# Kernel optimization log

Hardware: AMD Instinct MI355X
Metric: run time of the kernel (lower is better)

The kernel has to match this reference:

```python
import jax, jax.numpy as jnp
import numpy as np

NUM_GROUPS = 8
EPS = 1e-5


def group_norm(x, gamma, beta):
    # x: [B, C, H, W]
    B, C, H, W = x.shape
    xg = x.reshape(B, NUM_GROUPS, C // NUM_GROUPS, H, W)
    mean = xg.mean(axis=(2, 3, 4), keepdims=True)
    var = xg.var(axis=(2, 3, 4), keepdims=True)
    xn = ((xg - mean) * jax.lax.rsqrt(var + EPS)).reshape(B, C, H, W)
    return xn * gamma[None, :, None, None] + beta[None, :, None, None]


def conv1x1(x, w, b):
    # x: [B, C, H, W], w: [Cout, Cin], b: [Cout]
    return jnp.einsum('bchw,oc->bohw', x, w) + b[None, :, None, None]


def setup_inputs() -> dict:
    key = jax.random.key(0)
    ks = jax.random.split(key, 7)
    C = 128
    x = jax.random.normal(ks[0], (4, C, 64, 64), dtype=jnp.float32)
    norm_w = jnp.ones((C,), dtype=jnp.float32)
    norm_b = jnp.zeros((C,), dtype=jnp.float32)
    s = 1.0 / np.sqrt(C)
    qkv_w = jax.random.normal(ks[1], (3 * C, C), dtype=jnp.float32) * s
    qkv_b = jax.random.normal(ks[2], (3 * C,), dtype=jnp.float32) * 0.01
    proj_w = jax.random.normal(ks[3], (C, C), dtype=jnp.float32) * s
    proj_b = jax.random.normal(ks[4], (C,), dtype=jnp.float32) * 0.01
    return {"x": x, "norm_w": norm_w, "norm_b": norm_b,
            "qkv_w": qkv_w, "qkv_b": qkv_b,
            "proj_w": proj_w, "proj_b": proj_b}


def reference(x, norm_w, norm_b, qkv_w, qkv_b, proj_w, proj_b):
    B, C, H, W = x.shape
    qkv = conv1x1(group_norm(x, norm_w, norm_b), qkv_w, qkv_b)
    q, k, v = jnp.split(qkv, 3, axis=1)           # each [B, C, H, W]
    q = q.reshape(B, C, H * W).transpose(0, 2, 1)  # [B, HW, C]
    k = k.reshape(B, C, H * W)                     # [B, C, HW]
    v = v.reshape(B, C, H * W).transpose(0, 2, 1)  # [B, HW, C]
    scale = 1.0 / np.sqrt(C).astype(np.float32)
    attn = jax.nn.softmax(jnp.einsum('bnc,bcm->bnm', q, k) * scale, axis=-1)
    out = jnp.einsum('bnm,bmc->bnc', attn, v)      # [B, HW, C]
    out = out.transpose(0, 2, 1).reshape(B, C, H, W)
    return x + conv1x1(out, proj_w, proj_b)
```

## Files before the change

kernel.cpp:

```cpp
#include <hip/hip_runtime.h>

typedef unsigned short u16;
typedef unsigned int   u32;

#define HW 4096
#define NC 128

typedef __bf16 bf16x8 __attribute__((ext_vector_type(8)));
typedef float  f32x16 __attribute__((ext_vector_type(16)));

__device__ __forceinline__ bf16x8 as_bf8(uint4 u){
    union { uint4 u; bf16x8 b; } c; c.u = u; return c.b;
}
__device__ __forceinline__ u16 f2bf(float f){
    u32 u = __float_as_uint(f);
    return (u16)((u + 0x7fffu + ((u >> 16) & 1u)) >> 16);
}
__device__ __forceinline__ u32 pack2(float a, float b){
    return ((__float_as_uint(a) + 0x8000u) >> 16) | ((__float_as_uint(b) + 0x8000u) & 0xffff0000u);
}
__device__ __forceinline__ float bf_lo(u32 u){ return __uint_as_float(u << 16); }
__device__ __forceinline__ float bf_hi(u32 u){ return __uint_as_float(u & 0xffff0000u); }
__device__ __forceinline__ void unpack8(uint4 u, float* v){
    v[0]=bf_lo(u.x); v[1]=bf_hi(u.x); v[2]=bf_lo(u.y); v[3]=bf_hi(u.y);
    v[4]=bf_lo(u.z); v[5]=bf_hi(u.z); v[6]=bf_lo(u.w); v[7]=bf_hi(u.w);
}

#define GLOAD_LDS16(g, l) \
    __builtin_amdgcn_global_load_lds((const __attribute__((address_space(1))) u32*)(const void*)(g), \
                                     (__attribute__((address_space(3))) u32*)(void*)(l), 16, 0, 0)

__global__ __launch_bounds__(256) void gnw_kernel(const float* __restrict__ x,
                                                  float* __restrict__ stats,
                                                  const float* __restrict__ qkv_w,
                                                  const float* __restrict__ proj_w,
                                                  uint4* __restrict__ Wf,
                                                  uint4* __restrict__ Pf){
    if (blockIdx.x < 256){
        int bg = blockIdx.x >> 3, part = blockIdx.x & 7;
        const float4* p = (const float4*)(x + (size_t)bg * 65536 + part * 8192);
        float s = 0.f, ss = 0.f;
        #pragma unroll
        for (int i = 0; i < 8; i++){
            float4 u = p[threadIdx.x + i*256];
            s  += u.x + u.y + u.z + u.w;
            ss += u.x*u.x + u.y*u.y + u.z*u.z + u.w*u.w;
        }
        #pragma unroll
        for (int off = 32; off > 0; off >>= 1){
            s  += __shfl_xor(s,  off);
            ss += __shfl_xor(ss, off);
        }
        __shared__ float rs[4], rss[4];
        int wid = threadIdx.x >> 6;
        if ((threadIdx.x & 63) == 0){ rs[wid] = s; rss[wid] = ss; }
        __syncthreads();
        if (threadIdx.x == 0){
            stats[bg*16 + part*2]     = rs[0]+rs[1]+rs[2]+rs[3];
            stats[bg*16 + part*2 + 1] = rss[0]+rss[1]+rss[2]+rss[3];
        }
    } else {
        int id = (blockIdx.x - 256)*256 + threadIdx.x;
        const float* src; uint4* dst; int fi;
        if (id < 6144){ src = qkv_w; dst = Wf; fi = id; }
        else          { src = proj_w; dst = Pf; fi = id - 6144; }
        int l = fi & 63, ks = (fi >> 6) & 7, ob = fi >> 9;
        int o = ob*32 + (l & 31);
        int c = ks*16 + ((l >> 5) << 3);
        const float* s = src + o*128 + c;
        dst[fi] = make_uint4(pack2(s[0],s[1]), pack2(s[2],s[3]), pack2(s[4],s[5]), pack2(s[6],s[7]));
    }
}

__global__ __launch_bounds__(256) void qkv_kernel(const float* __restrict__ x,
                                                  const float* __restrict__ stats,
                                                  const float* __restrict__ gamma,
                                                  const float* __restrict__ beta,
                                                  const uint4* __restrict__ Wf,
                                                  const float* __restrict__ bias,
                                                  uint4* __restrict__ Qf,
                                                  uint4* __restrict__ Kf,
                                                  uint4* __restrict__ Vf){
    __shared__ float gaL[128], beL[128], biasL[384];
    int b = blockIdx.x >> 7, tokblk = blockIdx.x & 127;
    int t = threadIdx.x, lane = t & 63, wv = t >> 6;
    if (t < 128){
        int g = t >> 4;
        float S = 0.f, SS = 0.f;
        #pragma unroll
        for (int p = 0; p < 8; p++){
            S  += stats[(b*8 + g)*16 + p*2];
            SS += stats[(b*8 + g)*16 + p*2 + 1];
        }
        float mean = S * (1.f/65536.f);
        float rstd = rsqrtf(SS * (1.f/65536.f) - mean*mean + 1e-5f);
        float ga = gamma[t] * rstd;
        gaL[t] = ga; beL[t] = beta[t] - mean*ga;
    }
    if (t < 192){ biasL[t] = bias[t]; biasL[t+192] = bias[t+192]; }
    __syncthreads();

    int h = lane >> 5, tl = lane & 31;
    uint4 xf[8];
    const float* xb = x + (size_t)b*128*HW + tokblk*32 + tl;
    #pragma unroll
    for (int ks = 0; ks < 8; ks++){
        int c0 = ks*16 + h*8;
        float4 g0 = *(float4*)&gaL[c0], g1 = *(float4*)&gaL[c0+4];
        float4 e0 = *(float4*)&beL[c0], e1 = *(float4*)&beL[c0+4];
        float v[8];
        #pragma unroll
        for (int j = 0; j < 8; j++) v[j] = xb[(size_t)(c0+j)*HW];
        v[0] = fmaf(v[0], g0.x, e0.x); v[1] = fmaf(v[1], g0.y, e0.y);
        v[2] = fmaf(v[2], g0.z, e0.z); v[3] = fmaf(v[3], g0.w, e0.w);
        v[4] = fmaf(v[4], g1.x, e1.x); v[5] = fmaf(v[5], g1.y, e1.y);
        v[6] = fmaf(v[6], g1.z, e1.z); v[7] = fmaf(v[7], g1.w, e1.w);
        xf[ks] = make_uint4(pack2(v[0],v[1]), pack2(v[2],v[3]), pack2(v[4],v[5]), pack2(v[6],v[7]));
    }

    bool up = (lane >= 32);
    #pragma unroll
    for (int i = 0; i < 3; i++){
        int ob = wv*3 + i;
        uint4 wf[8];
        #pragma unroll
        for (int ks = 0; ks < 8; ks++) wf[ks] = Wf[(ob*8 + ks)*64 + lane];
        f32x16 D;
        #pragma unroll
        for (int r = 0; r < 16; r++) D[r] = 0.f;
        if (ob < 8){
            #pragma unroll
            for (int ks = 0; ks < 8; ks++)
                D = __builtin_amdgcn_mfma_f32_32x32x16_bf16(as_bf8(wf[ks]), as_bf8(xf[ks]), D, 0,0,0);
            #pragma unroll
            for (int r = 0; r < 16; r++)
                D[r] += biasL[ob*32 + (r&3) + 8*(r>>2) + 4*h];
            u32 pk[8], xch[8];
            #pragma unroll
            for (int j = 0; j < 8; j++) pk[j] = pack2(D[2*j], D[2*j+1]);
            #pragma unroll
            for (int j = 0; j < 8; j++) xch[j] = __shfl_xor(pk[j], 32);
            uint4 F0 = up ? make_uint4(xch[2],xch[3],pk[2],pk[3]) : make_uint4(pk[0],pk[1],xch[0],xch[1]);
            uint4 F1 = up ? make_uint4(xch[6],xch[7],pk[6],pk[7]) : make_uint4(pk[4],pk[5],xch[4],xch[5]);
            uint4* dst = (ob < 4) ? Qf : Kf;
            int obl = ob & 3;
            size_t base = (((size_t)b*128 + tokblk)*8 + obl*2)*64 + lane;
            dst[base] = F0; dst[base + 64] = F1;
        } else {
            #pragma unroll
            for (int ks = 0; ks < 8; ks++)
                D = __builtin_amdgcn_mfma_f32_32x32x16_bf16(as_bf8(xf[ks]), as_bf8(wf[ks]), D, 0,0,0);
            int nb = ob - 8;
            float vb = biasL[256 + nb*32 + tl];
            #pragma unroll
            for (int r = 0; r < 16; r++) D[r] += vb;
            u32 pk[8], xch[8];
            #pragma unroll
            for (int j = 0; j < 8; j++) pk[j] = pack2(D[2*j], D[2*j+1]);
            #pragma unroll
            for (int j = 0; j < 8; j++) xch[j] = __shfl_xor(pk[j], 32);
            uint4 F0 = up ? make_uint4(xch[2],xch[3],pk[2],pk[3]) : make_uint4(pk[0],pk[1],xch[0],xch[1]);
            uint4 F1 = up ? make_uint4(xch[6],xch[7],pk[6],pk[7]) : make_uint4(pk[4],pk[5],xch[4],xch[5]);
            int it = tokblk >> 1, t2 = tokblk & 1;
            size_t base = ((((size_t)b*64 + it)*4 + nb)*4 + t2*2)*64 + lane;
            Vf[base] = F0; Vf[base + 64] = F1;
        }
    }
}

__global__ __launch_bounds__(256, 2) void attn_kernel(const uint4* __restrict__ Qf,
                                                      const uint4* __restrict__ Kf,
                                                      const uint4* __restrict__ Vf,
                                                      u16* __restrict__ Opart,
                                                      float* __restrict__ lsum){
    __shared__ uint4 smem[2048];
    __shared__ float lred[64];
    int pair = blockIdx.x & 7, qx = blockIdx.x >> 3;
    int b = pair >> 1, ksp = pair & 1;
    int t = threadIdx.x, lane = t & 63, wv = t >> 6;
    int qh = wv >> 1, kh = wv & 1;
    const float SC = 0.08838834764831845f;

    uint4 qf[8];
    const uint4* qptr = Qf + ((size_t)b*128 + qx*2 + qh)*512 + lane;
    #pragma unroll
    for (int ks = 0; ks < 8; ks++) qf[ks] = qptr[ks*64];

    f32x16 O0, O1, O2, O3;
    #pragma unroll
    for (int r = 0; r < 16; r++){ O0[r]=0.f; O1[r]=0.f; O2[r]=0.f; O3[r]=0.f; }
    float l_i = 0.f;

    const uint4* kg = Kf + ((size_t)b*128 + ksp*64)*512;
    const uint4* vg = Vf + ((size_t)b*64  + ksp*32)*1024;

    #pragma unroll
    for (int i = 0; i < 4; i++)
        GLOAD_LDS16(kg + t + i*256, &smem[t + i*256]);
    __syncthreads();

    for (int it = 0; it < 32; it++){
        int cur = it & 1;
        if (it < 31){
            const uint4* kg2 = kg + (it+1)*1024;
            #pragma unroll
            for (int i = 0; i < 4; i++)
                GLOAD_LDS16(kg2 + t + i*256, &smem[(cur^1)*1024 + t + i*256]);
        }
        const uint4* vgi = vg + it*1024 + lane;
        uint4 vf[8];
        #pragma unroll
        for (int nb = 0; nb < 4; nb++){
            vf[nb*2]   = vgi[(nb*4 + kh*2)     << 6];
            vf[nb*2+1] = vgi[(nb*4 + kh*2 + 1) << 6];
        }

        f32x16 S0;
        #pragma unroll
        for (int r = 0; r < 16; r++) S0[r] = 0.f;
        #pragma unroll
        for (int ks = 0; ks < 8; ks++)
            S0 = __builtin_amdgcn_mfma_f32_32x32x16_bf16(
                     as_bf8(smem[cur*1024 + ((kh*8 + ks)<<6) + lane]),
                     as_bf8(qf[ks]), S0, 0,0,0);

        float psum = 0.f;
        u32 pk[8];
        #pragma unroll
        for (int q = 0; q < 4; q++){
            float e0 = __expf(__fmaf_rn(S0[q*4+0], SC, -8.f));
            float e1 = __expf(__fmaf_rn(S0[q*4+1], SC, -8.f));
            float e2 = __expf(__fmaf_rn(S0[q*4+2], SC, -8.f));
            float e3 = __expf(__fmaf_rn(S0[q*4+3], SC, -8.f));
            psum += (e0+e1)+(e2+e3);
            pk[2*q] = pack2(e0,e1); pk[2*q+1] = pack2(e2,e3);
        }
        psum += __shfl_xor(psum, 32);
        l_i += psum;

        u32 xch[8];
        #pragma unroll
        for (int i = 0; i < 8; i++) xch[i] = __shfl_xor(pk[i], 32);
        bool up = (lane >= 32);
        uint4 fr0 = up ? make_uint4(xch[2],xch[3],pk[2],pk[3]) : make_uint4(pk[0],pk[1],xch[0],xch[1]);
        uint4 fr1 = up ? make_uint4(xch[6],xch[7],pk[6],pk[7]) : make_uint4(pk[4],pk[5],xch[4],xch[5]);

        #pragma unroll
        for (int ks = 0; ks < 2; ks++){
            bf16x8 pa = as_bf8(ks ? fr1 : fr0);
            O0 = __builtin_amdgcn_mfma_f32_32x32x16_bf16(pa, as_bf8(vf[0*2+ks]), O0, 0,0,0);
            O1 = __builtin_amdgcn_mfma_f32_32x32x16_bf16(pa, as_bf8(vf[1*2+ks]), O1, 0,0,0);
            O2 = __builtin_amdgcn_mfma_f32_32x32x16_bf16(pa, as_bf8(vf[2*2+ks]), O2, 0,0,0);
            O3 = __builtin_amdgcn_mfma_f32_32x32x16_bf16(pa, as_bf8(vf[3*2+ks]), O3, 0,0,0);
        }
        __syncthreads();
    }

    float* fsm = (float*)smem;
    if (kh == 1){
        #pragma unroll
        for (int r = 0; r < 16; r++){
            fsm[((qh*4+0)*16 + r)*64 + lane] = O0[r];
            fsm[((qh*4+1)*16 + r)*64 + lane] = O1[r];
            fsm[((qh*4+2)*16 + r)*64 + lane] = O2[r];
            fsm[((qh*4+3)*16 + r)*64 + lane] = O3[r];
        }
        if (lane < 32) lred[qh*32 + lane] = l_i;
    }
    __syncthreads();
    if (kh == 0){
        float lt = l_i + lred[qh*32 + (lane & 31)];
        if (lane < 32) lsum[((size_t)(ksp*4 + b))*HW + qx*64 + qh*32 + lane] = lt;
        u16* ob = Opart + (((size_t)(ksp*4 + b))*HW + qx*64 + qh*32)*NC;
        #pragma unroll
        for (int r = 0; r < 16; r++){
            int qr = (r&3) + 8*(r>>2) + 4*(lane>>5);
            int c  = lane & 31;
            ob[qr*NC +      c] = f2bf(O0[r] + fsm[((qh*4+0)*16 + r)*64 + lane]);
            ob[qr*NC + 32 + c] = f2bf(O1[r] + fsm[((qh*4+1)*16 + r)*64 + lane]);
            ob[qr*NC + 64 + c] = f2bf(O2[r] + fsm[((qh*4+2)*16 + r)*64 + lane]);
            ob[qr*NC + 96 + c] = f2bf(O3[r] + fsm[((qh*4+3)*16 + r)*64 + lane]);
        }
    }
}

__global__ __launch_bounds__(256) void proj_kernel(const u16* __restrict__ Op,
                                                   const float* __restrict__ lsum,
                                                   const uint4* __restrict__ Pf,
                                                   const float* __restrict__ bias,
                                                   const float* __restrict__ x,
                                                   float* __restrict__ out){
    __shared__ float biasL[128];
    int t = threadIdx.x, lane = t & 63, wv = t >> 6;
    if (t < 128) biasL[t] = bias[t];
    __syncthreads();
    int b = blockIdx.x >> 6, tk = blockIdx.x & 63;
    int tokb2 = wv & 1, obh = wv >> 1;
    int tokblk = tk*2 + tokb2;
    int h = lane >> 5, tl = lane & 31;

    int rowg = b*HW + tokblk*32 + tl;
    float inv = 1.f / (lsum[rowg] + lsum[16384 + rowg]);
    const u16* p0 = Op + (size_t)rowg*NC + h*8;
    uint4 af[8];
    #pragma unroll
    for (int ks = 0; ks < 8; ks++){
        uint4 u0 = *(const uint4*)(p0 + ks*16);
        uint4 u1 = *(const uint4*)(p0 + 2097152 + ks*16);
        float v0[8], v1[8];
        unpack8(u0, v0); unpack8(u1, v1);
        u32 q[4];
        #pragma unroll
        for (int j = 0; j < 4; j++)
            q[j] = pack2((v0[2*j] + v1[2*j]) * inv, (v0[2*j+1] + v1[2*j+1]) * inv);
        af[ks] = make_uint4(q[0], q[1], q[2], q[3]);
    }

    #pragma unroll
    for (int i = 0; i < 2; i++){
        int ob = obh*2 + i;
        uint4 pf[8];
        #pragma unroll
        for (int ks = 0; ks < 8; ks++) pf[ks] = Pf[(ob*8 + ks)*64 + lane];
        f32x16 D;
        #pragma unroll
        for (int r = 0; r < 16; r++) D[r] = 0.f;
        #pragma unroll
        for (int ks = 0; ks < 8; ks++)
            D = __builtin_amdgcn_mfma_f32_32x32x16_bf16(as_bf8(pf[ks]), as_bf8(af[ks]), D, 0,0,0);
        #pragma unroll
        for (int r = 0; r < 16; r++){
            int o = ob*32 + (r&3) + 8*(r>>2) + 4*h;
            size_t gi = ((size_t)b*128 + o)*HW + tokblk*32 + tl;
            out[gi] = x[gi] + biasL[o] + D[r];
        }
    }
}

extern "C" void kernel_launch(void* const* d_in, const int* in_sizes, int n_in,
                              void* d_out, int out_size, void* d_ws, size_t ws_size,
                              hipStream_t stream){
    const float* x      = (const float*)d_in[0];
    const float* norm_w = (const float*)d_in[1];
    const float* norm_b = (const float*)d_in[2];
    const float* qkv_w  = (const float*)d_in[3];
    const float* qkv_b  = (const float*)d_in[4];
    const float* proj_w = (const float*)d_in[5];
    const float* proj_b = (const float*)d_in[6];
    float* out = (float*)d_out;

    char* w = (char*)d_ws;
    float* stats = (float*)w;
    uint4* Qf = (uint4*)(w + 2048);
    uint4* Kf = (uint4*)(w + 2048 + 4194304);
    uint4* Vf = (uint4*)(w + 2048 + 8388608);
    float* lsum = (float*)(w + 2048 + 12582912);
    uint4* Wf = (uint4*)(w + 2048 + 12582912 + 131072);
    uint4* Pf = (uint4*)(w + 2048 + 12582912 + 131072 + 98304);
    u16* Opart = (u16*)d_out;

    gnw_kernel<<<288, 256, 0, stream>>>(x, stats, qkv_w, proj_w, Wf, Pf);
    qkv_kernel<<<512, 256, 0, stream>>>(x, stats, norm_w, norm_b, Wf, qkv_b, Qf, Kf, Vf);
    attn_kernel<<<512, 256, 0, stream>>>(Qf, Kf, Vf, Opart, lsum);
    proj_kernel<<<256, 256, 0, stream>>>(Opart, lsum, Pf, proj_b, x, out);
}
```

Before: 141.0 us.

## Load K directly to registers, use exp2, and write fragment-layout partial outputs

The attention kernel drops the LDS double buffer for K and its per-iteration barrier. Each wave now loads its own K and V fragments straight into registers and prefetches the next tile after use. The QK accumulation is split into two independent MFMA chains, and the exponential uses the hardware exp2 with folded scale and bias constants. Partial outputs are written as packed MFMA-fragment uint4 tiles rather than scattered 16-bit stores, and the projection kernel reads them with coalesced vector loads. The cost is higher register pressure and exposed global-load latency without LDS staging.

Result: faster. 135.3 us (-4.0%).

```diff
diff --git a/kernel.cpp b/kernel.cpp
--- a/kernel.cpp
+++ b/kernel.cpp
@@ -26,9 +26,7 @@
     v[4]=bf_lo(u.z); v[5]=bf_hi(u.z); v[6]=bf_lo(u.w); v[7]=bf_hi(u.w);
 }
 
-#define GLOAD_LDS16(g, l) \
-    __builtin_amdgcn_global_load_lds((const __attribute__((address_space(1))) u32*)(const void*)(g), \
-                                     (__attribute__((address_space(3))) u32*)(void*)(l), 16, 0, 0)
+__device__ __forceinline__ float exp2_hw(float x){ return __builtin_amdgcn_exp2f(x); }
 
 __global__ __launch_bounds__(256) void gnw_kernel(const float* __restrict__ x,
                                                   float* __restrict__ stats,
@@ -171,67 +169,68 @@
 __global__ __launch_bounds__(256, 2) void attn_kernel(const uint4* __restrict__ Qf,
                                                       const uint4* __restrict__ Kf,
                                                       const uint4* __restrict__ Vf,
-                                                      u16* __restrict__ Opart,
+                                                      uint4* __restrict__ Opart,
                                                       float* __restrict__ lsum){
-    __shared__ uint4 smem[2048];
+    __shared__ float fsm[8192];
     __shared__ float lred[64];
     int pair = blockIdx.x & 7, qx = blockIdx.x >> 3;
     int b = pair >> 1, ksp = pair & 1;
     int t = threadIdx.x, lane = t & 63, wv = t >> 6;
     int qh = wv >> 1, kh = wv & 1;
-    const float SC = 0.08838834764831845f;
+    const float SC2 = 0.12751744361402804f;
+    const float B2  = -11.541560327111707f;
 
     uint4 qf[8];
-    const uint4* qptr = Qf + ((size_t)b*128 + qx*2 + qh)*512 + lane;
+    const uint4* qptr = Qf + (((size_t)b*128 + qx*2 + qh)*8)*64 + lane;
     #pragma unroll
     for (int ks = 0; ks < 8; ks++) qf[ks] = qptr[ks*64];
 
-    f32x16 O0, O1, O2, O3;
-    #pragma unroll
-    for (int r = 0; r < 16; r++){ O0[r]=0.f; O1[r]=0.f; O2[r]=0.f; O3[r]=0.f; }
+    f32x16 O[4];
+    #pragma unroll
+    for (int nb = 0; nb < 4; nb++)
+        #pragma unroll
+        for (int r = 0; r < 16; r++) O[nb][r] = 0.f;
     float l_i = 0.f;
 
-    const uint4* kg = Kf + ((size_t)b*128 + ksp*64)*512;
-    const uint4* vg = Vf + ((size_t)b*64  + ksp*32)*1024;
-
-    #pragma unroll
-    for (int i = 0; i < 4; i++)
-        GLOAD_LDS16(kg + t + i*256, &smem[t + i*256]);
-    __syncthreads();
+    const uint4* kgw = Kf + (((size_t)b*128 + ksp*64)*8)*64 + (kh<<9) + lane;
+    const uint4* vgw = Vf + (((size_t)b*64  + ksp*32)*16)*64 + (kh<<7) + lane;
+
+    uint4 kf[8], vf[8];
+    #pragma unroll
+    for (int ks = 0; ks < 8; ks++) kf[ks] = kgw[ks*64];
+    #pragma unroll
+    for (int nb = 0; nb < 4; nb++){
+        vf[nb*2]   = vgw[nb*256];
+        vf[nb*2+1] = vgw[nb*256 + 64];
+    }
 
     for (int it = 0; it < 32; it++){
-        int cur = it & 1;
+        f32x16 Sa, Sb;
+        #pragma unroll
+        for (int r = 0; r < 16; r++){ Sa[r] = 0.f; Sb[r] = 0.f; }
+        #pragma unroll
+        for (int ks = 0; ks < 4; ks++)
+            Sa = __builtin_amdgcn_mfma_f32_32x32x16_bf16(as_bf8(kf[ks]), as_bf8(qf[ks]), Sa, 0,0,0);
+        #pragma unroll
+        for (int ks = 4; ks < 8; ks++)
+            Sb = __builtin_amdgcn_mfma_f32_32x32x16_bf16(as_bf8(kf[ks]), as_bf8(qf[ks]), Sb, 0,0,0);
+        #pragma unroll
+        for (int r = 0; r < 16; r++) Sa[r] += Sb[r];
+
         if (it < 31){
-            const uint4* kg2 = kg + (it+1)*1024;
-            #pragma unroll
-            for (int i = 0; i < 4; i++)
-                GLOAD_LDS16(kg2 + t + i*256, &smem[(cur^1)*1024 + t + i*256]);
-        }
-        const uint4* vgi = vg + it*1024 + lane;
-        uint4 vf[8];
-        #pragma unroll
-        for (int nb = 0; nb < 4; nb++){
-            vf[nb*2]   = vgi[(nb*4 + kh*2)     << 6];
-            vf[nb*2+1] = vgi[(nb*4 + kh*2 + 1) << 6];
-        }
-
-        f32x16 S0;
-        #pragma unroll
-        for (int r = 0; r < 16; r++) S0[r] = 0.f;
-        #pragma unroll
-        for (int ks = 0; ks < 8; ks++)
-            S0 = __builtin_amdgcn_mfma_f32_32x32x16_bf16(
-                     as_bf8(smem[cur*1024 + ((kh*8 + ks)<<6) + lane]),
-                     as_bf8(qf[ks]), S0, 0,0,0);
+            const uint4* kn = kgw + (it+1)*1024;
+            #pragma unroll
+            for (int ks = 0; ks < 8; ks++) kf[ks] = kn[ks*64];
+        }
 
         float psum = 0.f;
         u32 pk[8];
         #pragma unroll
         for (int q = 0; q < 4; q++){
-            float e0 = __expf(__fmaf_rn(S0[q*4+0], SC, -8.f));
-            float e1 = __expf(__fmaf_rn(S0[q*4+1], SC, -8.f));
-            float e2 = __expf(__fmaf_rn(S0[q*4+2], SC, -8.f));
-            float e3 = __expf(__fmaf_rn(S0[q*4+3], SC, -8.f));
+            float e0 = exp2_hw(__fmaf_rn(Sa[q*4+0], SC2, B2));
+            float e1 = exp2_hw(__fmaf_rn(Sa[q*4+1], SC2, B2));
+            float e2 = exp2_hw(__fmaf_rn(Sa[q*4+2], SC2, B2));
+            float e3 = exp2_hw(__fmaf_rn(Sa[q*4+3], SC2, B2));
             psum += (e0+e1)+(e2+e3);
             pk[2*q] = pack2(e0,e1); pk[2*q+1] = pack2(e2,e3);
         }
@@ -246,45 +245,53 @@
         uint4 fr1 = up ? make_uint4(xch[6],xch[7],pk[6],pk[7]) : make_uint4(pk[4],pk[5],xch[4],xch[5]);
 
         #pragma unroll
-        for (int ks = 0; ks < 2; ks++){
-            bf16x8 pa = as_bf8(ks ? fr1 : fr0);
-            O0 = __builtin_amdgcn_mfma_f32_32x32x16_bf16(pa, as_bf8(vf[0*2+ks]), O0, 0,0,0);
-            O1 = __builtin_amdgcn_mfma_f32_32x32x16_bf16(pa, as_bf8(vf[1*2+ks]), O1, 0,0,0);
-            O2 = __builtin_amdgcn_mfma_f32_32x32x16_bf16(pa, as_bf8(vf[2*2+ks]), O2, 0,0,0);
-            O3 = __builtin_amdgcn_mfma_f32_32x32x16_bf16(pa, as_bf8(vf[3*2+ks]), O3, 0,0,0);
-        }
-        __syncthreads();
-    }
-
-    float* fsm = (float*)smem;
+        for (int nb = 0; nb < 4; nb++){
+            O[nb] = __builtin_amdgcn_mfma_f32_32x32x16_bf16(as_bf8(vf[nb*2]),   as_bf8(fr0), O[nb], 0,0,0);
+            O[nb] = __builtin_amdgcn_mfma_f32_32x32x16_bf16(as_bf8(vf[nb*2+1]), as_bf8(fr1), O[nb], 0,0,0);
+        }
+
+        if (it < 31){
+            const uint4* vn = vgw + (it+1)*1024;
+            #pragma unroll
+            for (int nb = 0; nb < 4; nb++){
+                vf[nb*2]   = vn[nb*256];
+                vf[nb*2+1] = vn[nb*256 + 64];
+            }
+        }
+    }
+
     if (kh == 1){
         #pragma unroll
-        for (int r = 0; r < 16; r++){
-            fsm[((qh*4+0)*16 + r)*64 + lane] = O0[r];
-            fsm[((qh*4+1)*16 + r)*64 + lane] = O1[r];
-            fsm[((qh*4+2)*16 + r)*64 + lane] = O2[r];
-            fsm[((qh*4+3)*16 + r)*64 + lane] = O3[r];
-        }
+        for (int nb = 0; nb < 4; nb++)
+            #pragma unroll
+            for (int r = 0; r < 16; r++)
+                fsm[((qh*4+nb)*16 + r)*64 + lane] = O[nb][r];
         if (lane < 32) lred[qh*32 + lane] = l_i;
     }
     __syncthreads();
     if (kh == 0){
         float lt = l_i + lred[qh*32 + (lane & 31)];
-        if (lane < 32) lsum[((size_t)(ksp*4 + b))*HW + qx*64 + qh*32 + lane] = lt;
-        u16* ob = Opart + (((size_t)(ksp*4 + b))*HW + qx*64 + qh*32)*NC;
-        #pragma unroll
-        for (int r = 0; r < 16; r++){
-            int qr = (r&3) + 8*(r>>2) + 4*(lane>>5);
-            int c  = lane & 31;
-            ob[qr*NC +      c] = f2bf(O0[r] + fsm[((qh*4+0)*16 + r)*64 + lane]);
-            ob[qr*NC + 32 + c] = f2bf(O1[r] + fsm[((qh*4+1)*16 + r)*64 + lane]);
-            ob[qr*NC + 64 + c] = f2bf(O2[r] + fsm[((qh*4+2)*16 + r)*64 + lane]);
-            ob[qr*NC + 96 + c] = f2bf(O3[r] + fsm[((qh*4+3)*16 + r)*64 + lane]);
-        }
-    }
-}
-
-__global__ __launch_bounds__(256) void proj_kernel(const u16* __restrict__ Op,
+        if (lane < 32) lsum[((size_t)(ksp*4 + b))*HW + (qx*2+qh)*32 + lane] = lt;
+        bool up = (lane >= 32);
+        uint4* oc = Opart + (size_t)ksp*262144 + (((size_t)b*128 + qx*2 + qh)*8)*64 + lane;
+        #pragma unroll
+        for (int nb = 0; nb < 4; nb++){
+            #pragma unroll
+            for (int r = 0; r < 16; r++) O[nb][r] += fsm[((qh*4+nb)*16 + r)*64 + lane];
+            u32 pk[8], xch[8];
+            #pragma unroll
+            for (int j = 0; j < 8; j++) pk[j] = pack2(O[nb][2*j], O[nb][2*j+1]);
+            #pragma unroll
+            for (int j = 0; j < 8; j++) xch[j] = __shfl_xor(pk[j], 32);
+            uint4 F0 = up ? make_uint4(xch[2],xch[3],pk[2],pk[3]) : make_uint4(pk[0],pk[1],xch[0],xch[1]);
+            uint4 F1 = up ? make_uint4(xch[6],xch[7],pk[6],pk[7]) : make_uint4(pk[4],pk[5],xch[4],xch[5]);
+            oc[(nb*2)*64]     = F0;
+            oc[(nb*2 + 1)*64] = F1;
+        }
+    }
+}
+
+__global__ __launch_bounds__(256) void proj_kernel(const uint4* __restrict__ Op,
                                                    const float* __restrict__ lsum,
                                                    const uint4* __restrict__ Pf,
                                                    const float* __restrict__ bias,
@@ -301,12 +308,12 @@
 
     int rowg = b*HW + tokblk*32 + tl;
     float inv = 1.f / (lsum[rowg] + lsum[16384 + rowg]);
-    const u16* p0 = Op + (size_t)rowg*NC + h*8;
+    const uint4* c0p = Op + (((size_t)b*128 + tokblk)*8)*64 + lane;
     uint4 af[8];
     #pragma unroll
     for (int ks = 0; ks < 8; ks++){
-        uint4 u0 = *(const uint4*)(p0 + ks*16);
-        uint4 u1 = *(const uint4*)(p0 + 2097152 + ks*16);
+        uint4 u0 = c0p[ks*64];
+        uint4 u1 = c0p[262144 + ks*64];
         float v0[8], v1[8];
         unpack8(u0, v0); unpack8(u1, v1);
         u32 q[4];
@@ -357,7 +364,7 @@
     float* lsum = (float*)(w + 2048 + 12582912);
     uint4* Wf = (uint4*)(w + 2048 + 12582912 + 131072);
     uint4* Pf = (uint4*)(w + 2048 + 12582912 + 131072 + 98304);
-    u16* Opart = (u16*)d_out;
+    uint4* Opart = (uint4*)d_out;
 
     gnw_kernel<<<288, 256, 0, stream>>>(x, stats, qkv_w, proj_w, Wf, Pf);
     qkv_kernel<<<512, 256, 0, stream>>>(x, stats, norm_w, norm_b, Wf, qkv_b, Qf, Kf, Vf);
```
